# Optimization experiments

Hardware: AMD Instinct MI355X
Metric: run time of the kernel (lower is better)

The kernel has to match this reference:

```python
import jax, jax.numpy as jnp
import numpy as np

EMB = 1024
HEADS = 16
HEAD_DIM = EMB // HEADS


def setup_inputs() -> dict:
    key = jax.random.key(0)
    ks = jax.random.split(key, 7)
    B, Sq, Sk = 4, 1024, 1024
    dp_emb = jax.random.normal(ks[0], (B, Sq, EMB), dtype=jnp.float32)
    dp_mask = jnp.ones((B, 1, 1, Sq), dtype=jnp.float32)
    K = jax.random.normal(ks[1], (B, HEADS, Sk, HEAD_DIM), dtype=jnp.float32)
    V = jax.random.normal(ks[2], (B, HEADS, Sk, HEAD_DIM), dtype=jnp.float32)
    M = jax.random.normal(ks[3], (B, HEADS, Sq, Sk), dtype=jnp.float32)
    # query Linear params (key/value Linears in the torch module are unused)
    Wq = jax.random.normal(ks[4], (EMB, EMB), dtype=jnp.float32) / np.sqrt(EMB)
    bq = jax.random.normal(ks[5], (EMB,), dtype=jnp.float32) * 0.01
    return {"dp_emb": dp_emb, "dp_mask": dp_mask, "K": K, "V": V, "M": M, "Wq": Wq, "bq": bq}


def reference(dp_emb, dp_mask, K, V, M, Wq, bq):
    B, Sq, E = dp_emb.shape
    H, d = HEADS, HEAD_DIM
    # query projection: nn.Linear -> x @ W.T + b
    q = dp_emb @ Wq.T + bq                                  # [B,Sq,E]
    q = q.reshape(B, Sq, H, d).transpose(0, 2, 1, 3)        # [B,H,Sq,d]
    scores = jnp.einsum('bhqd,bhkd->bhqk', q, K) / np.sqrt(d).astype(jnp.float32)
    scores = scores - M                                      # additive mask (subtraction)
    probs = jax.nn.softmax(scores, axis=-1)                  # [B,H,Sq,Sk]
    # (probs.T * dp_mask).T == probs * dp_mask reshaped to mask the query axis
    probs = probs * jnp.swapaxes(dp_mask, -1, -2)            # dp_mask [B,1,1,Sq] -> [B,1,Sq,1]
    target_score = jnp.sum(jnp.max(probs, axis=2), axis=1)   # [B,Sk]
    # dropout omitted (eval/inference semantics)
    ctx = jnp.einsum('bhqk,bhkd->bhqd', probs, V)            # [B,H,Sq,d]
    ctx = ctx.transpose(0, 2, 1, 3).reshape(B, Sq, E)
    return ctx, target_score
```

## Files before the change

kernel.cpp:

```cpp
#include <hip/hip_runtime.h>

#define B_ 4
#define H_ 16
#define SQ 1024
#define SK 1024
#define DHD 64
#define E_ 1024

typedef _Float16 half_t;
typedef __attribute__((ext_vector_type(8))) _Float16 half8;
typedef __attribute__((ext_vector_type(4))) _Float16 half4;
typedef __attribute__((ext_vector_type(4))) float f32x4;

static __device__ __forceinline__ f32x4 mfma16h(half8 a, half8 b, f32x4 c) {
  return __builtin_amdgcn_mfma_f32_16x16x32_f16(a, b, c, 0, 0, 0);
}
static __device__ __forceinline__ void lds_barrier() {
  asm volatile("s_waitcnt lgkmcnt(0)" ::: "memory");
  __builtin_amdgcn_s_barrier();
}

#define QW_BLOCKS 2560
__global__ __launch_bounds__(256) void prep_kernel(const float* __restrict__ emb,
                                                   const float* __restrict__ wq,
                                                   const float* __restrict__ K,
                                                   const float* __restrict__ V,
                                                   half_t* __restrict__ emb_h,
                                                   half_t* __restrict__ wq_h,
                                                   half_t* __restrict__ khn,
                                                   half_t* __restrict__ vt) {
  int bid = blockIdx.x, tid = threadIdx.x;
  if (bid < QW_BLOCKS) {
    int i = bid * 256 + tid;
    const float* src;
    half_t* dst;
    if (i < (B_ * SQ * E_ / 8)) {
      src = emb;
      dst = emb_h;
    } else {
      i -= B_ * SQ * E_ / 8;
      src = wq;
      dst = wq_h;
    }
    size_t off = (size_t)i * 8;
    f32x4 v0 = *(const f32x4*)(src + off);
    f32x4 v1 = *(const f32x4*)(src + off + 4);
    half8 h;
#pragma unroll
    for (int j = 0; j < 4; ++j) {
      h[j] = (half_t)v0[j];
      h[4 + j] = (half_t)v1[j];
    }
    *(half8*)(dst + off) = h;
    return;
  }
  bid -= QW_BLOCKS;
  int bh = bid >> 4, kt = bid & 15;
  const float* ks = K + ((size_t)bh * SK + kt * 64) * DHD;
  half_t* kd = khn + ((size_t)bh * SK + kt * 64) * DHD;
#pragma unroll
  for (int j = 0; j < 2; ++j) {
    int base = j * 2048 + tid * 8;
    f32x4 a = *(const f32x4*)(ks + base);
    f32x4 b = *(const f32x4*)(ks + base + 4);
    half8 h;
#pragma unroll
    for (int r = 0; r < 4; ++r) {
      h[r] = (half_t)(-a[r]);
      h[4 + r] = (half_t)(-b[r]);
    }
    *(half8*)(kd + base) = h;
  }
  __shared__ float tile[64][65];
  const float* vs = V + ((size_t)bh * SK + kt * 64) * DHD;
#pragma unroll
  for (int i = 0; i < 16; ++i) {
    int idx = i * 256 + tid;
    tile[idx >> 6][idx & 63] = vs[idx];
  }
  __syncthreads();
#pragma unroll
  for (int i = 0; i < 16; ++i) {
    int idx = i * 256 + tid;
    int d = idx >> 6, kk = idx & 63;
    vt[((size_t)bh * DHD + d) * SK + kt * 64 + kk] = (half_t)tile[kk][d];
  }
}

__global__ __launch_bounds__(256) void proj_kernel(const half_t* __restrict__ emb,
                                                   const half_t* __restrict__ wq,
                                                   const float* __restrict__ bq,
                                                   half_t* __restrict__ qh) {
  int bid = blockIdx.x;
  int xcd = bid & 7, jj = bid >> 3;
  int mt = xcd * 8 + (jj >> 4);
  int nt = jj & 15;
  int tid = threadIdx.x, wid = tid >> 6, lane = tid & 63;
  int lr = lane & 15, lg = lane >> 4;
  int m0 = mt * 64 + (wid >> 1) * 32;
  int n0 = nt * 64 + (wid & 1) * 32;
  f32x4 acc[2][2];
#pragma unroll
  for (int i = 0; i < 2; ++i)
#pragma unroll
    for (int j = 0; j < 2; ++j) acc[i][j] = (f32x4){0.f, 0.f, 0.f, 0.f};

  for (int kk = 0; kk < E_; kk += 32) {
    half8 a[2], b[2];
#pragma unroll
    for (int g = 0; g < 2; ++g) {
      a[g] = *(const half8*)(emb + (size_t)(m0 + g * 16 + lr) * E_ + kk + lg * 8);
      b[g] = *(const half8*)(wq + (size_t)(n0 + g * 16 + lr) * E_ + kk + lg * 8);
    }
#pragma unroll
    for (int i = 0; i < 2; ++i)
#pragma unroll
      for (int j = 0; j < 2; ++j) acc[i][j] = mfma16h(a[i], b[j], acc[i][j]);
  }
#pragma unroll
  for (int i = 0; i < 2; ++i)
#pragma unroll
    for (int j = 0; j < 2; ++j)
#pragma unroll
      for (int r = 0; r < 4; ++r) {
        int m = m0 + i * 16 + lg * 4 + r;
        int n = n0 + j * 16 + lr;
        float v = (acc[i][j][r] + bq[n]) * 0.180336880f;
        int b = m >> 10, sq = m & 1023, h = n >> 6, dd = n & 63;
        qh[((size_t)(b * H_ + h) * SQ + sq) * DHD + dd] = (half_t)v;
      }
}

__global__ __launch_bounds__(512, 4) void attn_kernel(const half_t* __restrict__ qh,
                                                      const half_t* __restrict__ khn,
                                                      const half_t* __restrict__ vt,
                                                      const float* __restrict__ M,
                                                      const float* __restrict__ dpm,
                                                      float* __restrict__ out,
                                                      float* __restrict__ pm) {
  __shared__ half_t panel[32][1032];
  __shared__ float rowscale[32];

  int bid = blockIdx.x;
  int x = bid & 7, j = bid >> 3;
  int bh = x * 8 + (j >> 5);
  int qt = j & 31;
  int q0 = qt << 5;
  int b = bh >> 4, h = bh & 15;

  int tid = threadIdx.x, wid = tid >> 6, lane = tid & 63;
  int lr = lane & 15, lg = lane >> 4;

  int qr = wid * 4 + lg;
  const float* mrow = M + ((size_t)bh * SQ + q0 + qr) * SK + lr * 4;
  f32x4 ms[16];
#pragma unroll
  for (int i = 0; i < 16; ++i) ms[i] = *(const f32x4*)(mrow + i * 64);
  __builtin_amdgcn_sched_barrier(0);

  const half_t* qbase = qh + ((size_t)bh * SQ + q0) * DHD;
  half8 aq[2][2];
#pragma unroll
  for (int qg = 0; qg < 2; ++qg)
#pragma unroll
    for (int dh = 0; dh < 2; ++dh)
      aq[qg][dh] = *(const half8*)(qbase + (size_t)(qg * 16 + lr) * DHD + dh * 32 + lg * 8);

  int kc0 = wid * 128;
#pragma unroll
  for (int kt = 0; kt < 8; ++kt) {
    const half_t* kr = khn + ((size_t)bh * SK + kc0 + kt * 16 + lr) * DHD + lg * 8;
    half8 k0 = *(const half8*)(kr);
    half8 k1 = *(const half8*)(kr + 32);
#pragma unroll
    for (int qg = 0; qg < 2; ++qg) {
      f32x4 T = (f32x4){0.f, 0.f, 0.f, 0.f};
      T = mfma16h(k0, aq[qg][0], T);
      T = mfma16h(k1, aq[qg][1], T);
      half4 ph;
#pragma unroll
      for (int r = 0; r < 4; ++r) ph[r] = (half_t)exp2f(-T[r]);
      *(half4*)&panel[qg * 16 + lr][kc0 + kt * 16 + lg * 4] = ph;
    }
  }
  lds_barrier();

  half_t* prow = &panel[qr][lr * 4];
  float rsum = 0.f;
#pragma unroll
  for (int i = 0; i < 16; ++i) {
    f32x4 m = ms[i];
    half4 es = *(const half4*)(prow + i * 64);
    half4 ph;
#pragma unroll
    for (int r = 0; r < 4; ++r) {
      float p = (float)es[r] * __expf(-m[r]);
      rsum += p;
      ph[r] = (half_t)p;
    }
    *(half4*)(prow + i * 64) = ph;
  }
  rsum += __shfl_xor(rsum, 1);
  rsum += __shfl_xor(rsum, 2);
  rsum += __shfl_xor(rsum, 4);
  rsum += __shfl_xor(rsum, 8);
  if (lr == 0) rowscale[qr] = dpm[b * SQ + q0 + qr] / rsum;
  lds_barrier();

  int qg = wid >> 2, d0 = (wid & 3) * 16;
  const half_t* vrow = vt + ((size_t)bh * DHD + d0 + lr) * SK;
  f32x4 acc = (f32x4){0.f, 0.f, 0.f, 0.f};
#pragma unroll 8
  for (int ks = 0; ks < SK; ks += 32) {
    half8 av = *(const half8*)(vrow + ks + lg * 8);
    half8 bp = *(const half8*)&panel[qg * 16 + lr][ks + lg * 8];
    acc = mfma16h(av, bp, acc);
  }
  float rs = rowscale[qg * 16 + lr];
  f32x4 res;
#pragma unroll
  for (int r = 0; r < 4; ++r) res[r] = acc[r] * rs;
  *(f32x4*)(out + ((size_t)b * SQ + q0 + qg * 16 + lr) * E_ + h * DHD + d0 + lg * 4) = res;

  {
    int c = tid * 2;
    float m0 = 0.f, m1 = 0.f;
#pragma unroll 8
    for (int r = 0; r < 32; ++r) {
      float w = rowscale[r];
      m0 = fmaxf(m0, (float)panel[r][c] * w);
      m1 = fmaxf(m1, (float)panel[r][c + 1] * w);
    }
    float* pmrow = pm + ((size_t)bh * 32 + qt) * SK + c;
    pmrow[0] = m0;
    pmrow[1] = m1;
  }
}

__global__ __launch_bounds__(256) void tscore_kernel(const float* __restrict__ pm,
                                                     float* __restrict__ out) {
  int bb = blockIdx.x;
  int b = bb >> 4, kq = bb & 15;
  int t = threadIdx.x;
  int kl = t & 63, hg = t >> 6;
  int k = kq * 64 + kl;
  float s = 0.f;
#pragma unroll
  for (int hh = hg * 4; hh < hg * 4 + 4; ++hh) {
    const float* p = pm + ((size_t)(b * H_ + hh) * 32) * SK + k;
    float mx = 0.f;
#pragma unroll
    for (int qt = 0; qt < 32; ++qt) mx = fmaxf(mx, p[(size_t)qt * SK]);
    s += mx;
  }
  __shared__ float red[4][64];
  red[hg][kl] = s;
  __syncthreads();
  if (t < 64)
    out[(size_t)B_ * SQ * E_ + b * SK + kq * 64 + t] =
        red[0][t] + red[1][t] + red[2][t] + red[3][t];
}

extern "C" void kernel_launch(void* const* d_in, const int* in_sizes, int n_in,
                              void* d_out, int out_size, void* d_ws, size_t ws_size,
                              hipStream_t stream) {
  const float* dp_emb = (const float*)d_in[0];
  const float* dp_mask = (const float*)d_in[1];
  const float* K = (const float*)d_in[2];
  const float* V = (const float*)d_in[3];
  const float* M = (const float*)d_in[4];
  const float* Wq = (const float*)d_in[5];
  const float* bq = (const float*)d_in[6];
  float* out = (float*)d_out;

  char* ws = (char*)d_ws;
  half_t* q_h = (half_t*)(ws);
  half_t* k_hn = (half_t*)(ws + (8ull << 20));
  half_t* vt_h = (half_t*)(ws + (16ull << 20));
  half_t* emb_h = (half_t*)(ws + (24ull << 20));
  half_t* wq_h = (half_t*)(ws + (32ull << 20));
  float* pm = (float*)(ws + (34ull << 20));

  prep_kernel<<<QW_BLOCKS + B_ * H_ * 16, 256, 0, stream>>>(dp_emb, Wq, K, V, emb_h, wq_h,
                                                            k_hn, vt_h);
  proj_kernel<<<1024, 256, 0, stream>>>(emb_h, wq_h, bq, q_h);
  attn_kernel<<<B_ * H_ * (SQ / 32), 512, 0, stream>>>(q_h, k_hn, vt_h, M, dp_mask, out, pm);
  tscore_kernel<<<64, 256, 0, stream>>>(pm, out);
}
```

Before: 213.2 us.

## Stream mask tiles through double-buffered LDS via async global_load_lds

Instead of holding the whole 32x1024 mask tile in registers (16 float4 per thread), the attention kernel now loads the mask in 256-column chunks straight into a double-buffered LDS staging area with global_load_lds. The loads overlap with the QK^T MFMA and exp work, and vmcnt waits step through the chunks. This frees a large block of registers, but the added LDS (about 67KB for mbuf alone) forces the occupancy hint down from 4 to 2 blocks per CU and adds barriers per chunk.

```diff
diff --git a/kernel.cpp b/kernel.cpp
--- a/kernel.cpp
+++ b/kernel.cpp
@@ -131,7 +131,7 @@
       }
 }
 
-__global__ __launch_bounds__(512, 4) void attn_kernel(const half_t* __restrict__ qh,
+__global__ __launch_bounds__(512, 2) void attn_kernel(const half_t* __restrict__ qh,
                                                       const half_t* __restrict__ khn,
                                                       const half_t* __restrict__ vt,
                                                       const float* __restrict__ M,
@@ -139,6 +139,7 @@
                                                       float* __restrict__ out,
                                                       float* __restrict__ pm) {
   __shared__ half_t panel[32][1032];
+  __shared__ float mbuf[2][32][264];
   __shared__ float rowscale[32];
 
   int bid = blockIdx.x;
@@ -151,60 +152,88 @@
   int tid = threadIdx.x, wid = tid >> 6, lane = tid & 63;
   int lr = lane & 15, lg = lane >> 4;
 
-  int qr = wid * 4 + lg;
-  const float* mrow = M + ((size_t)bh * SQ + q0 + qr) * SK + lr * 4;
-  f32x4 ms[16];
-#pragma unroll
-  for (int i = 0; i < 16; ++i) ms[i] = *(const f32x4*)(mrow + i * 64);
-  __builtin_amdgcn_sched_barrier(0);
-
-  const half_t* qbase = qh + ((size_t)bh * SQ + q0) * DHD;
-  half8 aq[2][2];
-#pragma unroll
-  for (int qg = 0; qg < 2; ++qg)
-#pragma unroll
-    for (int dh = 0; dh < 2; ++dh)
-      aq[qg][dh] = *(const half8*)(qbase + (size_t)(qg * 16 + lr) * DHD + dh * 32 + lg * 8);
-
-  int kc0 = wid * 128;
-#pragma unroll
-  for (int kt = 0; kt < 8; ++kt) {
-    const half_t* kr = khn + ((size_t)bh * SK + kc0 + kt * 16 + lr) * DHD + lg * 8;
-    half8 k0 = *(const half8*)(kr);
-    half8 k1 = *(const half8*)(kr + 32);
-#pragma unroll
-    for (int qg = 0; qg < 2; ++qg) {
-      f32x4 T = (f32x4){0.f, 0.f, 0.f, 0.f};
-      T = mfma16h(k0, aq[qg][0], T);
-      T = mfma16h(k1, aq[qg][1], T);
+  const float* mbase = M + ((size_t)bh * SQ + q0) * SK;
+
+#pragma unroll
+  for (int s = 0; s < 2; ++s)
+#pragma unroll
+    for (int i = 0; i < 4; ++i) {
+      int row = wid * 4 + i;
+      const float* g = mbase + (size_t)row * SK + s * 256 + lane * 4;
+      __builtin_amdgcn_global_load_lds(
+          (const __attribute__((address_space(1))) void*)g,
+          (__attribute__((address_space(3))) void*)&mbuf[s][row][0], 16, 0, 0);
+    }
+
+  {
+    const half_t* qbase = qh + ((size_t)bh * SQ + q0) * DHD;
+    half8 aq[2][2];
+#pragma unroll
+    for (int qg = 0; qg < 2; ++qg)
+#pragma unroll
+      for (int dh = 0; dh < 2; ++dh)
+        aq[qg][dh] =
+            *(const half8*)(qbase + (size_t)(qg * 16 + lr) * DHD + dh * 32 + lg * 8);
+    int kc0 = wid * 128;
+#pragma unroll
+    for (int kt = 0; kt < 8; ++kt) {
+      const half_t* kr = khn + ((size_t)bh * SK + kc0 + kt * 16 + lr) * DHD + lg * 8;
+      half8 k0 = *(const half8*)(kr);
+      half8 k1 = *(const half8*)(kr + 32);
+#pragma unroll
+      for (int qg = 0; qg < 2; ++qg) {
+        f32x4 T = (f32x4){0.f, 0.f, 0.f, 0.f};
+        T = mfma16h(k0, aq[qg][0], T);
+        T = mfma16h(k1, aq[qg][1], T);
+        half4 ph;
+#pragma unroll
+        for (int r = 0; r < 4; ++r) ph[r] = (half_t)exp2f(-T[r]);
+        *(half4*)&panel[qg * 16 + lr][kc0 + kt * 16 + lg * 4] = ph;
+      }
+    }
+  }
+
+  int qr = tid >> 4, sub = tid & 15;
+  float rsum = 0.f;
+#pragma unroll
+  for (int c = 0; c < 4; ++c) {
+    if (c < 3)
+      asm volatile("s_waitcnt vmcnt(4)" ::: "memory");
+    else
+      asm volatile("s_waitcnt vmcnt(0)" ::: "memory");
+    __builtin_amdgcn_sched_barrier(0);
+    lds_barrier();
+#pragma unroll
+    for (int jj = 0; jj < 4; ++jj) {
+      f32x4 m = *(const f32x4*)&mbuf[c & 1][qr][sub * 4 + jj * 64];
+      half4 es = *(const half4*)&panel[qr][c * 256 + sub * 4 + jj * 64];
       half4 ph;
 #pragma unroll
-      for (int r = 0; r < 4; ++r) ph[r] = (half_t)exp2f(-T[r]);
-      *(half4*)&panel[qg * 16 + lr][kc0 + kt * 16 + lg * 4] = ph;
-    }
-  }
-  lds_barrier();
-
-  half_t* prow = &panel[qr][lr * 4];
-  float rsum = 0.f;
-#pragma unroll
-  for (int i = 0; i < 16; ++i) {
-    f32x4 m = ms[i];
-    half4 es = *(const half4*)(prow + i * 64);
-    half4 ph;
-#pragma unroll
-    for (int r = 0; r < 4; ++r) {
-      float p = (float)es[r] * __expf(-m[r]);
-      rsum += p;
-      ph[r] = (half_t)p;
-    }
-    *(half4*)(prow + i * 64) = ph;
-  }
+      for (int r = 0; r < 4; ++r) {
+        float p = (float)es[r] * __expf(-m[r]);
+        rsum += p;
+        ph[r] = (half_t)p;
+      }
+      *(half4*)&panel[qr][c * 256 + sub * 4 + jj * 64] = ph;
+    }
+    lds_barrier();
+    if (c < 2) {
+#pragma unroll
+      for (int i = 0; i < 4; ++i) {
+        int row = wid * 4 + i;
+        const float* g = mbase + (size_t)row * SK + (c + 2) * 256 + lane * 4;
+        __builtin_amdgcn_global_load_lds(
+            (const __attribute__((address_space(1))) void*)g,
+            (__attribute__((address_space(3))) void*)&mbuf[c & 1][row][0], 16, 0, 0);
+      }
+    }
+  }
+
   rsum += __shfl_xor(rsum, 1);
   rsum += __shfl_xor(rsum, 2);
   rsum += __shfl_xor(rsum, 4);
   rsum += __shfl_xor(rsum, 8);
-  if (lr == 0) rowscale[qr] = dpm[b * SQ + q0 + qr] / rsum;
+  if (sub == 0) rowscale[qr] = dpm[b * SQ + q0 + qr] / rsum;
   lds_barrier();
 
   int qg = wid >> 2, d0 = (wid & 3) * 16;
```

New measurement: 239.7 us. +12.4%, slower.
